# Kernel optimization log

Hardware: AMD Instinct MI355X
Metric: run time of the kernel (lower is better)

The kernel has to match this reference:

```python
import jax, jax.numpy as jnp
import numpy as np
from jax import lax


def _maxpool_h(x):
    # MaxPool2d(kernel=(3,1), stride=(2,1), padding=(1,0)) on NCHW.
    # Torch pads with -inf for max pooling.
    return lax.reduce_window(
        x,
        -jnp.inf,
        lax.max,
        window_dimensions=(1, 1, 3, 1),
        window_strides=(1, 1, 2, 1),
        padding=((0, 0), (0, 0), (1, 1), (0, 0)),
    )


def setup_inputs() -> dict:
    key = jax.random.key(0)
    x = jax.random.normal(key, (32, 1, 8192, 256), dtype=jnp.float32)
    return {"x": x}


def reference(x) -> jnp.ndarray:
    out = _maxpool_h(x)  # [B, C, H', W]
    # Per-sample min-max normalization (vectorized over batch instead of the
    # original per-sample python loop).
    mx = jnp.max(out, axis=(1, 2, 3), keepdims=True)
    mn = jnp.min(out, axis=(1, 2, 3), keepdims=True)
    return (out - mn) / (mx - mn)
```

## Files before the change

### kernel.cpp

```cpp
#include <hip/hip_runtime.h>
#include <cfloat>

#define BATCH     32
#define H_IN      8192
#define H_OUT     4096
#define W         256
#define W4        64
#define CH        32
#define BLK_PER_B 32

typedef float f32x4 __attribute__((ext_vector_type(4)));

__device__ __forceinline__ float4 max3_f4(float4 a, float4 b, float4 c) {
    float4 m;
    m.x = fmaxf(a.x, fmaxf(b.x, c.x));
    m.y = fmaxf(a.y, fmaxf(b.y, c.y));
    m.z = fmaxf(a.z, fmaxf(b.z, c.z));
    m.w = fmaxf(a.w, fmaxf(b.w, c.w));
    return m;
}

__global__ __launch_bounds__(256) void pool_minmax(
        const float* __restrict__ x,
        float* __restrict__ partial_min, float* __restrict__ partial_max) {
    const int batch = blockIdx.x >> 5;
    const int blk   = blockIdx.x & 31;
    const int tid   = threadIdx.x;
    const int w4    = tid & 63;
    const int rg    = tid >> 6;
    const int h0    = blk * (BLK_PER_B * 4) + rg * CH;

    const float4* xin = (const float4*)x + (size_t)batch * H_IN * W4 + w4;

    float lmin = FLT_MAX, lmax = -FLT_MAX;

    float4 prev;
    const int r0 = 2 * h0 - 1;
    if (r0 >= 0) prev = xin[(size_t)r0 * W4];
    else         prev = make_float4(-FLT_MAX, -FLT_MAX, -FLT_MAX, -FLT_MAX);

    #pragma unroll 4
    for (int i = 0; i < CH; ++i) {
        const int r = 2 * (h0 + i);
        float4 a = xin[(size_t)r * W4];
        float4 c = xin[(size_t)(r + 1) * W4];
        float4 m = max3_f4(prev, a, c);
        prev = c;
        lmax = fmaxf(lmax, fmaxf(fmaxf(m.x, m.y), fmaxf(m.z, m.w)));
        lmin = fminf(lmin, fminf(fminf(m.x, m.y), fminf(m.z, m.w)));
    }

    #pragma unroll
    for (int off = 32; off > 0; off >>= 1) {
        lmax = fmaxf(lmax, __shfl_down(lmax, off, 64));
        lmin = fminf(lmin, __shfl_down(lmin, off, 64));
    }
    __shared__ float smax[4], smin[4];
    if ((tid & 63) == 0) { smax[rg] = lmax; smin[rg] = lmin; }
    __syncthreads();
    if (tid == 0) {
        float bmax = smax[0], bmin = smin[0];
        #pragma unroll
        for (int i = 1; i < 4; ++i) {
            bmax = fmaxf(bmax, smax[i]);
            bmin = fminf(bmin, smin[i]);
        }
        partial_max[blockIdx.x] = bmax;
        partial_min[blockIdx.x] = bmin;
    }
}

__global__ __launch_bounds__(256) void pool_normalize(
        const float* __restrict__ x, float* __restrict__ out,
        const float* __restrict__ pmin, const float* __restrict__ pmax) {
    const int batch = blockIdx.x >> 5;
    const int blk   = blockIdx.x & 31;
    const int tid   = threadIdx.x;

    __shared__ float s_mn, s_inv;
    if (tid < 64) {
        float mn = (tid < BLK_PER_B) ? pmin[batch * BLK_PER_B + tid] : FLT_MAX;
        float mx = (tid < BLK_PER_B) ? pmax[batch * BLK_PER_B + tid] : -FLT_MAX;
        #pragma unroll
        for (int off = 16; off > 0; off >>= 1) {
            mn = fminf(mn, __shfl_down(mn, off, 64));
            mx = fmaxf(mx, __shfl_down(mx, off, 64));
        }
        if (tid == 0) { s_mn = mn; s_inv = 1.0f / (mx - mn); }
    }
    __syncthreads();
    const float mn  = s_mn;
    const float inv = s_inv;

    const int w4 = tid & 63;
    const int rg = tid >> 6;
    const int h0 = blk * (BLK_PER_B * 4) + rg * CH;

    const float4* xin = (const float4*)x + (size_t)batch * H_IN * W4 + w4;
    f32x4*        po  = (f32x4*)out + ((size_t)batch * H_OUT + h0) * W4 + w4;

    float4 prev;
    const int r0 = 2 * h0 - 1;
    if (r0 >= 0) prev = xin[(size_t)r0 * W4];
    else         prev = make_float4(-FLT_MAX, -FLT_MAX, -FLT_MAX, -FLT_MAX);

    #pragma unroll 4
    for (int i = 0; i < CH; ++i) {
        const int r = 2 * (h0 + i);
        float4 a = xin[(size_t)r * W4];
        float4 c = xin[(size_t)(r + 1) * W4];
        float4 m = max3_f4(prev, a, c);
        prev = c;
        f32x4 v = { (m.x - mn) * inv,
                    (m.y - mn) * inv,
                    (m.z - mn) * inv,
                    (m.w - mn) * inv };
        __builtin_nontemporal_store(v, po + (size_t)i * W4);
    }
}

extern "C" void kernel_launch(void* const* d_in, const int* in_sizes, int n_in,
                              void* d_out, int out_size, void* d_ws, size_t ws_size,
                              hipStream_t stream) {
    const float* x   = (const float*)d_in[0];
    float*       out = (float*)d_out;
    float*       ws  = (float*)d_ws;

    float* pmin = ws;
    float* pmax = ws + 1024;

    pool_minmax<<<BATCH * BLK_PER_B, 256, 0, stream>>>(x, pmin, pmax);
    pool_normalize<<<BATCH * BLK_PER_B, 256, 0, stream>>>(x, out, pmin, pmax);
}
```

Measured before the change: 436.7 us.

## Store pooled output in first pass, normalize in place in second pass

The first kernel now writes the unnormalized pooled result to the output while it computes per-block min and max. The second kernel reads that pooled buffer back and rescales it in place, instead of re-reading the input and redoing the pooling. The input is twice the size of the output, so the second pass's read traffic is halved and it has a better chance of being served from the large last-level cache. The grid is also doubled by halving the rows each block handles, which adds parallelism. The cost is an extra write of the intermediate in the first pass, so total bytes moved stay about the same.

```diff
diff --git a/kernel.cpp b/kernel.cpp
--- a/kernel.cpp
+++ b/kernel.cpp
@@ -6,8 +6,8 @@
 #define H_OUT     4096
 #define W         256
 #define W4        64
-#define CH        32
-#define BLK_PER_B 32
+#define CH        16
+#define BLK_PER_B 64
 
 typedef float f32x4 __attribute__((ext_vector_type(4)));
 
@@ -20,17 +20,18 @@
     return m;
 }
 
-__global__ __launch_bounds__(256) void pool_minmax(
-        const float* __restrict__ x,
+__global__ __launch_bounds__(256) void pool_store_partial(
+        const float* __restrict__ x, float* __restrict__ out,
         float* __restrict__ partial_min, float* __restrict__ partial_max) {
-    const int batch = blockIdx.x >> 5;
-    const int blk   = blockIdx.x & 31;
+    const int batch = blockIdx.x >> 6;
+    const int blk   = blockIdx.x & 63;
     const int tid   = threadIdx.x;
     const int w4    = tid & 63;
     const int rg    = tid >> 6;
-    const int h0    = blk * (BLK_PER_B * 4) + rg * CH;
+    const int h0    = blk * (4 * CH) + rg * CH;
 
     const float4* xin = (const float4*)x + (size_t)batch * H_IN * W4 + w4;
+    float4*       po  = (float4*)out + ((size_t)batch * H_OUT + h0) * W4 + w4;
 
     float lmin = FLT_MAX, lmax = -FLT_MAX;
 
@@ -45,6 +46,7 @@
         float4 a = xin[(size_t)r * W4];
         float4 c = xin[(size_t)(r + 1) * W4];
         float4 m = max3_f4(prev, a, c);
+        po[(size_t)i * W4] = m;
         prev = c;
         lmax = fmaxf(lmax, fmaxf(fmaxf(m.x, m.y), fmaxf(m.z, m.w)));
         lmin = fminf(lmin, fminf(fminf(m.x, m.y), fminf(m.z, m.w)));
@@ -70,19 +72,19 @@
     }
 }
 
-__global__ __launch_bounds__(256) void pool_normalize(
-        const float* __restrict__ x, float* __restrict__ out,
+__global__ __launch_bounds__(256) void finish_normalize(
+        float* __restrict__ out,
         const float* __restrict__ pmin, const float* __restrict__ pmax) {
-    const int batch = blockIdx.x >> 5;
-    const int blk   = blockIdx.x & 31;
+    const int batch = blockIdx.x >> 6;
+    const int blk   = blockIdx.x & 63;
     const int tid   = threadIdx.x;
 
     __shared__ float s_mn, s_inv;
     if (tid < 64) {
-        float mn = (tid < BLK_PER_B) ? pmin[batch * BLK_PER_B + tid] : FLT_MAX;
-        float mx = (tid < BLK_PER_B) ? pmax[batch * BLK_PER_B + tid] : -FLT_MAX;
+        float mn = pmin[batch * BLK_PER_B + tid];
+        float mx = pmax[batch * BLK_PER_B + tid];
         #pragma unroll
-        for (int off = 16; off > 0; off >>= 1) {
+        for (int off = 32; off > 0; off >>= 1) {
             mn = fminf(mn, __shfl_down(mn, off, 64));
             mx = fmaxf(mx, __shfl_down(mx, off, 64));
         }
@@ -92,30 +94,16 @@
     const float mn  = s_mn;
     const float inv = s_inv;
 
-    const int w4 = tid & 63;
-    const int rg = tid >> 6;
-    const int h0 = blk * (BLK_PER_B * 4) + rg * CH;
-
-    const float4* xin = (const float4*)x + (size_t)batch * H_IN * W4 + w4;
-    f32x4*        po  = (f32x4*)out + ((size_t)batch * H_OUT + h0) * W4 + w4;
-
-    float4 prev;
-    const int r0 = 2 * h0 - 1;
-    if (r0 >= 0) prev = xin[(size_t)r0 * W4];
-    else         prev = make_float4(-FLT_MAX, -FLT_MAX, -FLT_MAX, -FLT_MAX);
-
+    f32x4* p = (f32x4*)out + (size_t)batch * (H_OUT * W4) + (size_t)blk * 4096;
     #pragma unroll 4
-    for (int i = 0; i < CH; ++i) {
-        const int r = 2 * (h0 + i);
-        float4 a = xin[(size_t)r * W4];
-        float4 c = xin[(size_t)(r + 1) * W4];
-        float4 m = max3_f4(prev, a, c);
-        prev = c;
-        f32x4 v = { (m.x - mn) * inv,
-                    (m.y - mn) * inv,
-                    (m.z - mn) * inv,
-                    (m.w - mn) * inv };
-        __builtin_nontemporal_store(v, po + (size_t)i * W4);
+    for (int j = 0; j < 16; ++j) {
+        const int idx = tid + j * 256;
+        f32x4 v = p[idx];
+        v.x = (v.x - mn) * inv;
+        v.y = (v.y - mn) * inv;
+        v.z = (v.z - mn) * inv;
+        v.w = (v.w - mn) * inv;
+        __builtin_nontemporal_store(v, p + idx);
     }
 }
 
@@ -127,8 +115,8 @@
     float*       ws  = (float*)d_ws;
 
     float* pmin = ws;
-    float* pmax = ws + 1024;
+    float* pmax = ws + 2048;
 
-    pool_minmax<<<BATCH * BLK_PER_B, 256, 0, stream>>>(x, pmin, pmax);
-    pool_normalize<<<BATCH * BLK_PER_B, 256, 0, stream>>>(x, out, pmin, pmax);
+    pool_store_partial<<<BATCH * BLK_PER_B, 256, 0, stream>>>(x, out, pmin, pmax);
+    finish_normalize<<<BATCH * BLK_PER_B, 256, 0, stream>>>(out, pmin, pmax);
 }
```

New measurement: 427.1 us. 1.02x faster.
